# Kernel tuning notes

Hardware: AMD Instinct MI355X
Metric: run time of the kernel (lower is better)

The kernel has to match this reference:

```python
import jax, jax.numpy as jnp
import numpy as np

MODES = (16, 16, 16)

def setup_inputs() -> dict:
    key = jax.random.key(0)
    k1, k2, k3 = jax.random.split(key, 3)
    B, Cin, Cout = 4, 64, 64
    D = H = W = 64
    x = jax.random.normal(k1, (B, Cin, D, H, W), dtype=jnp.float32)
    weights = jax.random.normal(k2, (Cin, Cout) + MODES, dtype=jnp.float32) * (1.0 / (Cin * Cout)) ** 0.5
    bias = jax.random.normal(k3, (Cout,), dtype=jnp.float32)
    return {"x": x, "weights": weights, "bias": bias}


def reference(x, weights, bias):
    B = x.shape[0]
    Cout = weights.shape[1]
    spatial = x.shape[-3:]
    # 3D real FFT over last three dims -> (B, Cin, D, H, W//2+1) complex
    x_ft = jnp.fft.rfftn(x, axes=(-3, -2, -1))
    m1 = min(MODES[0], x_ft.shape[-3])
    m2 = min(MODES[1], x_ft.shape[-2])
    m3 = min(MODES[2], x_ft.shape[-1])
    # Per-mode channel mixing on truncated low-frequency block: one batched complex einsum
    mixed = jnp.einsum(
        'bixyz,ioxyz->boxyz',
        x_ft[:, :, :m1, :m2, :m3],
        weights[:, :, :m1, :m2, :m3],
    )
    out_ft = jnp.zeros((B, Cout) + x_ft.shape[2:], dtype=x_ft.dtype)
    out_ft = out_ft.at[:, :, :m1, :m2, :m3].set(mixed)
    x_out = jnp.fft.irfftn(out_ft, s=spatial, axes=(-3, -2, -1))
    return x_out + bias[None, :, None, None, None]
```

## Files before the change

### kernel.cpp

```cpp
#include <hip/hip_runtime.h>


#define ANG 0.09817477042468103f
#define C1W 0.9951847266721969f
#define S1W 0.0980171403295606f

__global__ __launch_bounds__(256) void k_fwd_hw(const float* __restrict__ x,
                                                float2* __restrict__ T1) {
  __shared__ float xs[64][68];
  __shared__ float2 irc[64][17];
  const int t = threadIdx.x;
  const int blk = blockIdx.x;
  const float* xg = x + (size_t)blk * 4096;
#pragma unroll
  for (int j = 0; j < 4; ++j) {
    int v = j * 256 + t;
    float4 val = reinterpret_cast<const float4*>(xg)[v];
    *reinterpret_cast<float4*>(&xs[v >> 4][(v & 15) * 4]) = val;
  }
  __syncthreads();
  {
    const int k = t & 15;
    const int g = t >> 4;
    float s1, c1;
    sincosf(ANG * (float)k, &s1, &c1);
    s1 = -s1;
    const float c2 = c1 * c1 - s1 * s1;
    const float s2 = 2.f * c1 * s1;
    float cw = 1.f, sw = 0.f;
    float ar0=0,ai0=0,ar1=0,ai1=0,ar2=0,ai2=0,ar3=0,ai3=0;
    const float2* r0 = reinterpret_cast<const float2*>(&xs[4*g+0][0]);
    const float2* r1 = reinterpret_cast<const float2*>(&xs[4*g+1][0]);
    const float2* r2 = reinterpret_cast<const float2*>(&xs[4*g+2][0]);
    const float2* r3 = reinterpret_cast<const float2*>(&xs[4*g+3][0]);
#pragma unroll 8
    for (int w2 = 0; w2 < 32; ++w2) {
      float2 v0 = r0[w2], v1 = r1[w2], v2 = r2[w2], v3 = r3[w2];
      float co = cw * c1 - sw * s1;
      float so = sw * c1 + cw * s1;
      ar0 = fmaf(v0.x, cw, ar0); ai0 = fmaf(v0.x, sw, ai0);
      ar1 = fmaf(v1.x, cw, ar1); ai1 = fmaf(v1.x, sw, ai1);
      ar2 = fmaf(v2.x, cw, ar2); ai2 = fmaf(v2.x, sw, ai2);
      ar3 = fmaf(v3.x, cw, ar3); ai3 = fmaf(v3.x, sw, ai3);
      ar0 = fmaf(v0.y, co, ar0); ai0 = fmaf(v0.y, so, ai0);
      ar1 = fmaf(v1.y, co, ar1); ai1 = fmaf(v1.y, so, ai1);
      ar2 = fmaf(v2.y, co, ar2); ai2 = fmaf(v2.y, so, ai2);
      ar3 = fmaf(v3.y, co, ar3); ai3 = fmaf(v3.y, so, ai3);
      float nc = cw * c2 - sw * s2;
      sw = sw * c2 + cw * s2;
      cw = nc;
    }
    irc[4*g+0][k] = make_float2(ar0, ai0);
    irc[4*g+1][k] = make_float2(ar1, ai1);
    irc[4*g+2][k] = make_float2(ar2, ai2);
    irc[4*g+3][k] = make_float2(ar3, ai3);
  }
  __syncthreads();
  {
    const int kz = t & 15, ky = t >> 4;
    float s1, c1;
    sincosf(ANG * (float)ky, &s1, &c1);
    s1 = -s1;
    float cw = 1.f, sw = 0.f, ar = 0.f, ai = 0.f;
#pragma unroll 8
    for (int r = 0; r < 64; ++r) {
      float2 v = irc[r][kz];
      ar += v.x * cw - v.y * sw;
      ai += v.y * cw + v.x * sw;
      float nc = cw * c1 - sw * s1;
      sw = sw * c1 + cw * s1;
      cw = nc;
    }
    T1[(size_t)blk * 256 + t] = make_float2(ar, ai);
  }
}

__global__ __launch_bounds__(256) void k_fwd_d(const float2* __restrict__ T1,
                                               float2* __restrict__ T2) {
  __shared__ float2 tw[64];
  const int t = threadIdx.x;
  if (t < 64) {
    float s, c; sincosf(ANG * (float)t, &s, &c);
    tw[t] = make_float2(c, s);
  }
  __syncthreads();
  const int bi = blockIdx.x;
  const float2* src = T1 + (size_t)bi * 16384 + t;
  float ar[16], ai[16];
#pragma unroll
  for (int q = 0; q < 16; ++q) { ar[q] = 0.f; ai[q] = 0.f; }
#pragma unroll 4
  for (int d = 0; d < 64; ++d) {
    float2 v = src[(size_t)d * 256];
    int m = 0;
#pragma unroll
    for (int kx = 0; kx < 16; ++kx) {
      float2 w = tw[m];
      ar[kx] = fmaf(v.x, w.x, fmaf(v.y, w.y, ar[kx]));
      ai[kx] = fmaf(v.y, w.x, fmaf(-v.x, w.y, ai[kx]));
      m = (m + d) & 63;
    }
  }
  float2* dst = T2 + (size_t)bi * 4096 + t;
#pragma unroll
  for (int kx = 0; kx < 16; ++kx)
    dst[(size_t)kx * 256] = make_float2(ar[kx], ai[kx]);
}

__global__ __launch_bounds__(256) void k_mix(const float2* __restrict__ T2,
                                             const float* __restrict__ wgt,
                                             float2* __restrict__ MX) {
  const int t = threadIdx.x;
  const int b = blockIdx.x >> 6;
  const int mode = ((blockIdx.x & 63) << 6) + (t & 63);
  const int og = t >> 6;
  const float2* xin = T2 + (size_t)b * 64 * 4096;
  float accr[16], acci[16];
#pragma unroll
  for (int j = 0; j < 16; ++j) { accr[j] = 0.f; acci[j] = 0.f; }
  for (int i = 0; i < 64; ++i) {
    float2 xv = xin[(size_t)i * 4096 + mode];
    const float* wp = wgt + ((size_t)i * 64 + og * 16) * 4096 + mode;
#pragma unroll
    for (int j = 0; j < 16; ++j) {
      float wv = wp[(size_t)j * 4096];
      accr[j] = fmaf(xv.x, wv, accr[j]);
      acci[j] = fmaf(xv.y, wv, acci[j]);
    }
  }
  float2* outp = MX + (size_t)b * 64 * 4096 + mode;
#pragma unroll
  for (int j = 0; j < 16; ++j)
    outp[(size_t)(og * 16 + j) * 4096] = make_float2(accr[j], acci[j]);
}

__global__ __launch_bounds__(256) void k_inv(const float2* __restrict__ MX,
                                             const float* __restrict__ bias,
                                             float* __restrict__ out) {
  __shared__ float2 tw[64];
  __shared__ float2 inb[16][17];
  __shared__ float2 g2[64][17];
  const int t = threadIdx.x;
  const int blk = blockIdx.x;
  const int d = blk & 63;
  const int bo = blk >> 6;
  if (t < 64) {
    float s, c; sincosf(ANG * (float)t, &s, &c);
    tw[t] = make_float2(c, s);
  }
  __syncthreads();
  {
    const float2* src = MX + (size_t)bo * 4096 + t;
    float ar = 0.f, ai = 0.f;
    int m = 0;
#pragma unroll
    for (int kx = 0; kx < 16; ++kx) {
      float2 v = src[(size_t)kx * 256];
      float2 w = tw[m];
      ar += v.x * w.x - v.y * w.y;
      ai += v.x * w.y + v.y * w.x;
      m = (m + d) & 63;
    }
    inb[t >> 4][t & 15] = make_float2(ar, ai);
  }
  __syncthreads();
  {
    const int kz = t & 15, g = t >> 4;
    const int h0 = 4 * g;
    float ar[4] = {0,0,0,0}, ai[4] = {0,0,0,0};
    int m0 = 0, m1 = 0, m2 = 0, m3 = 0;
#pragma unroll
    for (int ky = 0; ky < 16; ++ky) {
      float2 v = inb[ky][kz];
      float2 w0 = tw[m0], w1 = tw[m1], w2 = tw[m2], w3 = tw[m3];
      ar[0] += v.x*w0.x - v.y*w0.y; ai[0] += v.x*w0.y + v.y*w0.x;
      ar[1] += v.x*w1.x - v.y*w1.y; ai[1] += v.x*w1.y + v.y*w1.x;
      ar[2] += v.x*w2.x - v.y*w2.y; ai[2] += v.x*w2.y + v.y*w2.x;
      ar[3] += v.x*w3.x - v.y*w3.y; ai[3] += v.x*w3.y + v.y*w3.x;
      m0 = (m0 + h0    ) & 63; m1 = (m1 + h0 + 1) & 63;
      m2 = (m2 + h0 + 2) & 63; m3 = (m3 + h0 + 3) & 63;
    }
#pragma unroll
    for (int j = 0; j < 4; ++j)
      g2[h0 + j][kz] = make_float2(ar[j] + ar[j], ai[j] + ai[j]);
  }
  __syncthreads();
  {
    const int wq = t & 15, hg = t >> 4;
    const int w0 = wq * 4;
    float s0, c0;
    sincosf(ANG * (float)w0, &s0, &c0);
    float stc[4], sts[4];
    stc[0] = c0; sts[0] = s0;
    stc[1] = stc[0]*C1W - sts[0]*S1W; sts[1] = sts[0]*C1W + stc[0]*S1W;
    stc[2] = stc[1]*C1W - sts[1]*S1W; sts[2] = sts[1]*C1W + stc[1]*S1W;
    stc[3] = stc[2]*C1W - sts[2]*S1W; sts[3] = sts[2]*C1W + stc[2]*S1W;
    float chc[4], chs[4];
    float acc[4][4];
#pragma unroll
    for (int wi = 0; wi < 4; ++wi) { chc[wi] = stc[wi]; chs[wi] = sts[wi]; }
#pragma unroll
    for (int j = 0; j < 4; ++j) {
      float dc = 0.5f * g2[4*hg + j][0].x;
#pragma unroll
      for (int wi = 0; wi < 4; ++wi) acc[j][wi] = dc;
    }
#pragma unroll
    for (int kk = 1; kk < 16; ++kk) {
      float2 gv0 = g2[4*hg + 0][kk];
      float2 gv1 = g2[4*hg + 1][kk];
      float2 gv2 = g2[4*hg + 2][kk];
      float2 gv3 = g2[4*hg + 3][kk];
#pragma unroll
      for (int wi = 0; wi < 4; ++wi) {
        float c = chc[wi], s = chs[wi];
        acc[0][wi] = fmaf(gv0.x, c, fmaf(-gv0.y, s, acc[0][wi]));
        acc[1][wi] = fmaf(gv1.x, c, fmaf(-gv1.y, s, acc[1][wi]));
        acc[2][wi] = fmaf(gv2.x, c, fmaf(-gv2.y, s, acc[2][wi]));
        acc[3][wi] = fmaf(gv3.x, c, fmaf(-gv3.y, s, acc[3][wi]));
      }
#pragma unroll
      for (int wi = 0; wi < 4; ++wi) {
        float nc = chc[wi]*stc[wi] - chs[wi]*sts[wi];
        chs[wi] = chs[wi]*stc[wi] + chc[wi]*sts[wi];
        chc[wi] = nc;
      }
    }
    const float bv = bias[bo & 63];
    const float scale = 3.814697265625e-06f;
    float* og = out + (size_t)blk * 4096;
#pragma unroll
    for (int j = 0; j < 4; ++j) {
      float4 res;
      res.x = fmaf(acc[j][0], scale, bv);
      res.y = fmaf(acc[j][1], scale, bv);
      res.z = fmaf(acc[j][2], scale, bv);
      res.w = fmaf(acc[j][3], scale, bv);
      *reinterpret_cast<float4*>(og + (4*hg + j) * 64 + w0) = res;
    }
  }
}

extern "C" void kernel_launch(void* const* d_in, const int* in_sizes, int n_in,
                              void* d_out, int out_size, void* d_ws, size_t ws_size,
                              hipStream_t stream) {
  const float* x    = (const float*)d_in[0];
  const float* wgt  = (const float*)d_in[1];
  const float* bias = (const float*)d_in[2];
  float* out = (float*)d_out;

  float* wsf = (float*)d_ws;
  float2* T1 = (float2*)wsf;
  float2* T2 = (float2*)(wsf + 8388608);
  float2* MX = (float2*)(wsf + 8388608 + 2097152);

  k_fwd_hw<<<16384, 256, 0, stream>>>(x, T1);
  k_fwd_d <<<256,   256, 0, stream>>>(T1, T2);
  k_mix   <<<256,   256, 0, stream>>>(T2, wgt, MX);
  k_inv   <<<16384, 256, 0, stream>>>(MX, bias, out);
}
```

Baseline: 700.6 us.

## Restructure all four kernels with symmetry-folded DFTs and radix-4 splits

Result: faster. 647.8 us (-7.5%).

```diff
diff --git a/kernel.cpp b/kernel.cpp
--- a/kernel.cpp
+++ b/kernel.cpp
@@ -2,15 +2,18 @@
 
 
 #define ANG 0.09817477042468103f
-#define C1W 0.9951847266721969f
-#define S1W 0.0980171403295606f
 
 __global__ __launch_bounds__(256) void k_fwd_hw(const float* __restrict__ x,
                                                 float2* __restrict__ T1) {
   __shared__ float xs[64][68];
+  __shared__ float xpm[64][68];
   __shared__ float2 irc[64][17];
+  __shared__ float2 tw[64];
+  float2 (*U)[16][17] = reinterpret_cast<float2(*)[16][17]>(&xs[0][0]);
+
   const int t = threadIdx.x;
   const int blk = blockIdx.x;
+  if (t < 64) { float s, c; sincosf(ANG * (float)t, &s, &c); tw[t] = make_float2(c, s); }
   const float* xg = x + (size_t)blk * 4096;
 #pragma unroll
   for (int j = 0; j < 4; ++j) {
@@ -19,57 +22,79 @@
     *reinterpret_cast<float4*>(&xs[v >> 4][(v & 15) * 4]) = val;
   }
   __syncthreads();
-  {
-    const int k = t & 15;
-    const int g = t >> 4;
-    float s1, c1;
-    sincosf(ANG * (float)k, &s1, &c1);
-    s1 = -s1;
-    const float c2 = c1 * c1 - s1 * s1;
-    const float s2 = 2.f * c1 * s1;
-    float cw = 1.f, sw = 0.f;
-    float ar0=0,ai0=0,ar1=0,ai1=0,ar2=0,ai2=0,ar3=0,ai3=0;
-    const float2* r0 = reinterpret_cast<const float2*>(&xs[4*g+0][0]);
-    const float2* r1 = reinterpret_cast<const float2*>(&xs[4*g+1][0]);
-    const float2* r2 = reinterpret_cast<const float2*>(&xs[4*g+2][0]);
-    const float2* r3 = reinterpret_cast<const float2*>(&xs[4*g+3][0]);
-#pragma unroll 8
-    for (int w2 = 0; w2 < 32; ++w2) {
-      float2 v0 = r0[w2], v1 = r1[w2], v2 = r2[w2], v3 = r3[w2];
-      float co = cw * c1 - sw * s1;
-      float so = sw * c1 + cw * s1;
-      ar0 = fmaf(v0.x, cw, ar0); ai0 = fmaf(v0.x, sw, ai0);
-      ar1 = fmaf(v1.x, cw, ar1); ai1 = fmaf(v1.x, sw, ai1);
-      ar2 = fmaf(v2.x, cw, ar2); ai2 = fmaf(v2.x, sw, ai2);
-      ar3 = fmaf(v3.x, cw, ar3); ai3 = fmaf(v3.x, sw, ai3);
-      ar0 = fmaf(v0.y, co, ar0); ai0 = fmaf(v0.y, so, ai0);
-      ar1 = fmaf(v1.y, co, ar1); ai1 = fmaf(v1.y, so, ai1);
-      ar2 = fmaf(v2.y, co, ar2); ai2 = fmaf(v2.y, so, ai2);
-      ar3 = fmaf(v3.y, co, ar3); ai3 = fmaf(v3.y, so, ai3);
-      float nc = cw * c2 - sw * s2;
-      sw = sw * c2 + cw * s2;
-      cw = nc;
-    }
-    irc[4*g+0][k] = make_float2(ar0, ai0);
-    irc[4*g+1][k] = make_float2(ar1, ai1);
-    irc[4*g+2][k] = make_float2(ar2, ai2);
-    irc[4*g+3][k] = make_float2(ar3, ai3);
-  }
-  __syncthreads();
-  {
-    const int kz = t & 15, ky = t >> 4;
-    float s1, c1;
-    sincosf(ANG * (float)ky, &s1, &c1);
-    s1 = -s1;
-    float cw = 1.f, sw = 0.f, ar = 0.f, ai = 0.f;
-#pragma unroll 8
-    for (int r = 0; r < 64; ++r) {
-      float2 v = irc[r][kz];
-      ar += v.x * cw - v.y * sw;
-      ai += v.y * cw + v.x * sw;
-      float nc = cw * c1 - sw * s1;
-      sw = sw * c1 + cw * s1;
-      cw = nc;
+#pragma unroll
+  for (int p = 0; p < 8; ++p) {
+    int f = p * 256 + t;
+    int row = f >> 5, w = f & 31;
+    if (w == 0) { xpm[row][63] = xs[row][0]; xpm[row][64] = xs[row][32]; }
+    else {
+      float a = xs[row][w], b2 = xs[row][64 - w];
+      xpm[row][w - 1] = a + b2;
+      xpm[row][31 + w] = a - b2;
+    }
+  }
+  __syncthreads();
+  {
+    const int k = t & 15, g = t >> 4;
+    const int r0 = 4 * g;
+    const float x32sign = (k & 1) ? -1.f : 1.f;
+    float re[4], im[4];
+#pragma unroll
+    for (int j = 0; j < 4; ++j) {
+      re[j] = fmaf(x32sign, xpm[r0 + j][64], xpm[r0 + j][63]);
+      im[j] = 0.f;
+    }
+#pragma unroll 5
+    for (int i = 0; i < 15; ++i) {
+      int w = 2 * i + 1;
+      float2 tw1 = tw[(k * w) & 63];
+      float2 tw2 = tw[(k * (w + 1)) & 63];
+#pragma unroll
+      for (int j = 0; j < 4; ++j) {
+        float2 xp = *reinterpret_cast<const float2*>(&xpm[r0 + j][w - 1]);
+        float2 xm = *reinterpret_cast<const float2*>(&xpm[r0 + j][31 + w]);
+        re[j] = fmaf(xp.x, tw1.x, re[j]); im[j] = fmaf(xm.x, tw1.y, im[j]);
+        re[j] = fmaf(xp.y, tw2.x, re[j]); im[j] = fmaf(xm.y, tw2.y, im[j]);
+      }
+    }
+    {
+      float2 tw1 = tw[(k * 31) & 63];
+#pragma unroll
+      for (int j = 0; j < 4; ++j) {
+        re[j] = fmaf(xpm[r0 + j][30], tw1.x, re[j]);
+        im[j] = fmaf(xpm[r0 + j][62], tw1.y, im[j]);
+      }
+    }
+#pragma unroll
+    for (int j = 0; j < 4; ++j) irc[r0 + j][k] = make_float2(re[j], -im[j]);
+  }
+  __syncthreads();
+  {
+    const int rho = t >> 4, kz = t & 15;
+    float2 v0 = irc[rho][kz], v1 = irc[rho + 16][kz];
+    float2 v2 = irc[rho + 32][kz], v3 = irc[rho + 48][kz];
+    float t0r = v0.x + v2.x, t0i = v0.y + v2.y;
+    float t1r = v0.x - v2.x, t1i = v0.y - v2.y;
+    float t2r = v1.x + v3.x, t2i = v1.y + v3.y;
+    float t3r = v1.x - v3.x, t3i = v1.y - v3.y;
+    U[0][rho][kz] = make_float2(t0r + t2r, t0i + t2i);
+    U[2][rho][kz] = make_float2(t0r - t2r, t0i - t2i);
+    U[1][rho][kz] = make_float2(t1r + t3i, t1i - t3r);
+    U[3][rho][kz] = make_float2(t1r - t3i, t1i + t3r);
+  }
+  __syncthreads();
+  {
+    const int ky = t >> 4, kz = t & 15;
+    const int m = ky & 3;
+    float ar = 0.f, ai = 0.f;
+    int idx = 0;
+#pragma unroll
+    for (int rho = 0; rho < 16; ++rho) {
+      float2 wv = tw[idx];
+      float2 u = U[m][rho][kz];
+      ar = fmaf(u.x, wv.x, fmaf(u.y, wv.y, ar));
+      ai = fmaf(u.y, wv.x, fmaf(-u.x, wv.y, ai));
+      idx = (idx + ky) & 63;
     }
     T1[(size_t)blk * 256 + t] = make_float2(ar, ai);
   }
@@ -77,61 +102,71 @@
 
 __global__ __launch_bounds__(256) void k_fwd_d(const float2* __restrict__ T1,
                                                float2* __restrict__ T2) {
+  __shared__ float2 s1[64][17];
   __shared__ float2 tw[64];
   const int t = threadIdx.x;
-  if (t < 64) {
-    float s, c; sincosf(ANG * (float)t, &s, &c);
-    tw[t] = make_float2(c, s);
-  }
-  __syncthreads();
-  const int bi = blockIdx.x;
-  const float2* src = T1 + (size_t)bi * 16384 + t;
-  float ar[16], ai[16];
-#pragma unroll
-  for (int q = 0; q < 16; ++q) { ar[q] = 0.f; ai[q] = 0.f; }
-#pragma unroll 4
+  if (t < 64) { float s, c; sincosf(ANG * (float)t, &s, &c); tw[t] = make_float2(c, s); }
+  const int bi = blockIdx.x >> 4, ky = blockIdx.x & 15;
+  const float2* src = T1 + (size_t)bi * 16384 + ky * 16;
+#pragma unroll
+  for (int p = 0; p < 4; ++p) {
+    int j = p * 256 + t;
+    s1[j >> 4][j & 15] = src[(size_t)(j >> 4) * 256 + (j & 15)];
+  }
+  __syncthreads();
+  const int kx = t >> 4, kz = t & 15;
+  float ar = 0.f, ai = 0.f;
+  int idx = 0;
+#pragma unroll 8
   for (int d = 0; d < 64; ++d) {
-    float2 v = src[(size_t)d * 256];
-    int m = 0;
-#pragma unroll
-    for (int kx = 0; kx < 16; ++kx) {
-      float2 w = tw[m];
-      ar[kx] = fmaf(v.x, w.x, fmaf(v.y, w.y, ar[kx]));
-      ai[kx] = fmaf(v.y, w.x, fmaf(-v.x, w.y, ai[kx]));
-      m = (m + d) & 63;
-    }
-  }
-  float2* dst = T2 + (size_t)bi * 4096 + t;
-#pragma unroll
-  for (int kx = 0; kx < 16; ++kx)
-    dst[(size_t)kx * 256] = make_float2(ar[kx], ai[kx]);
+    float2 v = s1[d][kz];
+    float2 wv = tw[idx];
+    ar = fmaf(v.x, wv.x, fmaf(v.y, wv.y, ar));
+    ai = fmaf(v.y, wv.x, fmaf(-v.x, wv.y, ai));
+    idx = (idx + kx) & 63;
+  }
+  T2[(size_t)bi * 4096 + kx * 256 + ky * 16 + kz] = make_float2(ar, ai);
 }
 
 __global__ __launch_bounds__(256) void k_mix(const float2* __restrict__ T2,
                                              const float* __restrict__ wgt,
                                              float2* __restrict__ MX) {
-  const int t = threadIdx.x;
-  const int b = blockIdx.x >> 6;
-  const int mode = ((blockIdx.x & 63) << 6) + (t & 63);
-  const int og = t >> 6;
-  const float2* xin = T2 + (size_t)b * 64 * 4096;
-  float accr[16], acci[16];
-#pragma unroll
-  for (int j = 0; j < 16; ++j) { accr[j] = 0.f; acci[j] = 0.f; }
+  __shared__ float2 ts2[4][64][8];
+  const int t = threadIdx.x;
+  const int mbase = blockIdx.x * 8;
+#pragma unroll
+  for (int p = 0; p < 8; ++p) {
+    int j = p * 256 + t;
+    int m = j & 7, i = (j >> 3) & 63, b = j >> 9;
+    ts2[b][i][m] = T2[(size_t)(b * 64 + i) * 4096 + mbase + m];
+  }
+  __syncthreads();
+  const int b = t >> 6, o = t & 63;
+  float accr[8], acci[8];
+#pragma unroll
+  for (int m = 0; m < 8; ++m) { accr[m] = 0.f; acci[m] = 0.f; }
+  const float* wp0 = wgt + (size_t)o * 4096 + mbase;
+#pragma unroll 2
   for (int i = 0; i < 64; ++i) {
-    float2 xv = xin[(size_t)i * 4096 + mode];
-    const float* wp = wgt + ((size_t)i * 64 + og * 16) * 4096 + mode;
-#pragma unroll
-    for (int j = 0; j < 16; ++j) {
-      float wv = wp[(size_t)j * 4096];
-      accr[j] = fmaf(xv.x, wv, accr[j]);
-      acci[j] = fmaf(xv.y, wv, acci[j]);
-    }
-  }
-  float2* outp = MX + (size_t)b * 64 * 4096 + mode;
-#pragma unroll
-  for (int j = 0; j < 16; ++j)
-    outp[(size_t)(og * 16 + j) * 4096] = make_float2(accr[j], acci[j]);
+    const float* wp = wp0 + (size_t)i * 262144;
+    float4 wa = *reinterpret_cast<const float4*>(wp);
+    float4 wb = *reinterpret_cast<const float4*>(wp + 4);
+    const float4* xv = reinterpret_cast<const float4*>(&ts2[b][i][0]);
+    float4 x0 = xv[0], x1 = xv[1], x2 = xv[2], x3 = xv[3];
+    accr[0] = fmaf(x0.x, wa.x, accr[0]); acci[0] = fmaf(x0.y, wa.x, acci[0]);
+    accr[1] = fmaf(x0.z, wa.y, accr[1]); acci[1] = fmaf(x0.w, wa.y, acci[1]);
+    accr[2] = fmaf(x1.x, wa.z, accr[2]); acci[2] = fmaf(x1.y, wa.z, acci[2]);
+    accr[3] = fmaf(x1.z, wa.w, accr[3]); acci[3] = fmaf(x1.w, wa.w, acci[3]);
+    accr[4] = fmaf(x2.x, wb.x, accr[4]); acci[4] = fmaf(x2.y, wb.x, acci[4]);
+    accr[5] = fmaf(x2.z, wb.y, accr[5]); acci[5] = fmaf(x2.w, wb.y, acci[5]);
+    accr[6] = fmaf(x3.x, wb.z, accr[6]); acci[6] = fmaf(x3.y, wb.z, acci[6]);
+    accr[7] = fmaf(x3.z, wb.w, accr[7]); acci[7] = fmaf(x3.w, wb.w, acci[7]);
+  }
+  float4* outp = reinterpret_cast<float4*>(MX + (size_t)(b * 64 + o) * 4096 + mbase);
+  outp[0] = make_float4(accr[0], acci[0], accr[1], acci[1]);
+  outp[1] = make_float4(accr[2], acci[2], accr[3], acci[3]);
+  outp[2] = make_float4(accr[4], acci[4], accr[5], acci[5]);
+  outp[3] = make_float4(accr[6], acci[6], accr[7], acci[7]);
 }
 
 __global__ __launch_bounds__(256) void k_inv(const float2* __restrict__ MX,
@@ -142,101 +177,86 @@
   __shared__ float2 g2[64][17];
   const int t = threadIdx.x;
   const int blk = blockIdx.x;
-  const int d = blk & 63;
-  const int bo = blk >> 6;
-  if (t < 64) {
-    float s, c; sincosf(ANG * (float)t, &s, &c);
-    tw[t] = make_float2(c, s);
-  }
+  const int d = blk & 63, bo = blk >> 6;
+  if (t < 64) { float s, c; sincosf(ANG * (float)t, &s, &c); tw[t] = make_float2(c, s); }
   __syncthreads();
   {
     const float2* src = MX + (size_t)bo * 4096 + t;
     float ar = 0.f, ai = 0.f;
-    int m = 0;
+    int idx = 0;
 #pragma unroll
     for (int kx = 0; kx < 16; ++kx) {
       float2 v = src[(size_t)kx * 256];
-      float2 w = tw[m];
-      ar += v.x * w.x - v.y * w.y;
-      ai += v.x * w.y + v.y * w.x;
-      m = (m + d) & 63;
+      float2 wv = tw[idx];
+      ar = fmaf(v.x, wv.x, fmaf(-v.y, wv.y, ar));
+      ai = fmaf(v.x, wv.y, fmaf(v.y, wv.x, ai));
+      idx = (idx + d) & 63;
     }
     inb[t >> 4][t & 15] = make_float2(ar, ai);
   }
   __syncthreads();
   {
-    const int kz = t & 15, g = t >> 4;
-    const int h0 = 4 * g;
-    float ar[4] = {0,0,0,0}, ai[4] = {0,0,0,0};
-    int m0 = 0, m1 = 0, m2 = 0, m3 = 0;
+    const int j = t >> 4, kz = t & 15;
+    float2 S[4];
+#pragma unroll
+    for (int q = 0; q < 4; ++q) S[q] = make_float2(0.f, 0.f);
+    int idx = 0;
 #pragma unroll
     for (int ky = 0; ky < 16; ++ky) {
+      float2 wv = tw[idx];
       float2 v = inb[ky][kz];
-      float2 w0 = tw[m0], w1 = tw[m1], w2 = tw[m2], w3 = tw[m3];
-      ar[0] += v.x*w0.x - v.y*w0.y; ai[0] += v.x*w0.y + v.y*w0.x;
-      ar[1] += v.x*w1.x - v.y*w1.y; ai[1] += v.x*w1.y + v.y*w1.x;
-      ar[2] += v.x*w2.x - v.y*w2.y; ai[2] += v.x*w2.y + v.y*w2.x;
-      ar[3] += v.x*w3.x - v.y*w3.y; ai[3] += v.x*w3.y + v.y*w3.x;
-      m0 = (m0 + h0    ) & 63; m1 = (m1 + h0 + 1) & 63;
-      m2 = (m2 + h0 + 2) & 63; m3 = (m3 + h0 + 3) & 63;
-    }
-#pragma unroll
-    for (int j = 0; j < 4; ++j)
-      g2[h0 + j][kz] = make_float2(ar[j] + ar[j], ai[j] + ai[j]);
-  }
-  __syncthreads();
-  {
-    const int wq = t & 15, hg = t >> 4;
-    const int w0 = wq * 4;
-    float s0, c0;
-    sincosf(ANG * (float)w0, &s0, &c0);
-    float stc[4], sts[4];
-    stc[0] = c0; sts[0] = s0;
-    stc[1] = stc[0]*C1W - sts[0]*S1W; sts[1] = sts[0]*C1W + stc[0]*S1W;
-    stc[2] = stc[1]*C1W - sts[1]*S1W; sts[2] = sts[1]*C1W + stc[1]*S1W;
-    stc[3] = stc[2]*C1W - sts[2]*S1W; sts[3] = sts[2]*C1W + stc[2]*S1W;
-    float chc[4], chs[4];
-    float acc[4][4];
-#pragma unroll
-    for (int wi = 0; wi < 4; ++wi) { chc[wi] = stc[wi]; chs[wi] = sts[wi]; }
-#pragma unroll
-    for (int j = 0; j < 4; ++j) {
-      float dc = 0.5f * g2[4*hg + j][0].x;
-#pragma unroll
-      for (int wi = 0; wi < 4; ++wi) acc[j][wi] = dc;
-    }
-#pragma unroll
-    for (int kk = 1; kk < 16; ++kk) {
-      float2 gv0 = g2[4*hg + 0][kk];
-      float2 gv1 = g2[4*hg + 1][kk];
-      float2 gv2 = g2[4*hg + 2][kk];
-      float2 gv3 = g2[4*hg + 3][kk];
-#pragma unroll
-      for (int wi = 0; wi < 4; ++wi) {
-        float c = chc[wi], s = chs[wi];
-        acc[0][wi] = fmaf(gv0.x, c, fmaf(-gv0.y, s, acc[0][wi]));
-        acc[1][wi] = fmaf(gv1.x, c, fmaf(-gv1.y, s, acc[1][wi]));
-        acc[2][wi] = fmaf(gv2.x, c, fmaf(-gv2.y, s, acc[2][wi]));
-        acc[3][wi] = fmaf(gv3.x, c, fmaf(-gv3.y, s, acc[3][wi]));
-      }
-#pragma unroll
-      for (int wi = 0; wi < 4; ++wi) {
-        float nc = chc[wi]*stc[wi] - chs[wi]*sts[wi];
-        chs[wi] = chs[wi]*stc[wi] + chc[wi]*sts[wi];
-        chc[wi] = nc;
-      }
+      S[ky & 3].x = fmaf(v.x, wv.x, fmaf(-v.y, wv.y, S[ky & 3].x));
+      S[ky & 3].y = fmaf(v.x, wv.y, fmaf(v.y, wv.x, S[ky & 3].y));
+      idx = (idx + j) & 63;
+    }
+    float t0r = S[0].x + S[2].x, t0i = S[0].y + S[2].y;
+    float t1r = S[0].x - S[2].x, t1i = S[0].y - S[2].y;
+    float t2r = S[1].x + S[3].x, t2i = S[1].y + S[3].y;
+    float t3r = S[1].x - S[3].x, t3i = S[1].y - S[3].y;
+    float f = (kz == 0) ? 1.f : 2.f;
+    g2[j     ][kz] = make_float2(f * (t0r + t2r), f * (t0i + t2i));
+    g2[j + 16][kz] = make_float2(f * (t1r - t3i), f * (t1i + t3r));
+    g2[j + 32][kz] = make_float2(f * (t0r - t2r), f * (t0i - t2i));
+    g2[j + 48][kz] = make_float2(f * (t1r + t3i), f * (t1i - t3r));
+  }
+  __syncthreads();
+  {
+    const int b = t & 15, hg = t >> 4;
+    float twc[16], tws[16];
+    int idx = 0;
+#pragma unroll
+    for (int k = 0; k < 16; ++k) {
+      float2 wv = tw[idx];
+      twc[k] = wv.x; tws[k] = wv.y;
+      idx = (idx + b) & 63;
     }
     const float bv = bias[bo & 63];
     const float scale = 3.814697265625e-06f;
     float* og = out + (size_t)blk * 4096;
 #pragma unroll
-    for (int j = 0; j < 4; ++j) {
-      float4 res;
-      res.x = fmaf(acc[j][0], scale, bv);
-      res.y = fmaf(acc[j][1], scale, bv);
-      res.z = fmaf(acc[j][2], scale, bv);
-      res.w = fmaf(acc[j][3], scale, bv);
-      *reinterpret_cast<float4*>(og + (4*hg + j) * 64 + w0) = res;
+    for (int j2 = 0; j2 < 4; ++j2) {
+      const int h = 4 * hg + j2;
+      float S0r = 0.f, S2r = 0.f, S1r = 0.f, S1i = 0.f, S3r = 0.f, S3i = 0.f;
+#pragma unroll
+      for (int k = 0; k < 16; ++k) {
+        float2 g = g2[h][k];
+        float pr = fmaf(g.x, twc[k], -g.y * tws[k]);
+        if ((k & 1) == 0) {
+          if ((k & 3) == 0) S0r += pr; else S2r += pr;
+        } else {
+          float pi = fmaf(g.x, tws[k], g.y * twc[k]);
+          if ((k & 3) == 1) { S1r += pr; S1i += pi; }
+          else              { S3r += pr; S3i += pi; }
+        }
+      }
+      float e0 = S0r + S2r;
+      float e1 = S0r - S2r;
+      float e2 = S1r + S3r;
+      float e3 = S1i - S3i;
+      og[h * 64 + b     ] = fmaf(e0 + e2, scale, bv);
+      og[h * 64 + b + 16] = fmaf(e1 - e3, scale, bv);
+      og[h * 64 + b + 32] = fmaf(e0 - e2, scale, bv);
+      og[h * 64 + b + 48] = fmaf(e1 + e3, scale, bv);
     }
   }
 }
@@ -255,7 +275,7 @@
   float2* MX = (float2*)(wsf + 8388608 + 2097152);
 
   k_fwd_hw<<<16384, 256, 0, stream>>>(x, T1);
-  k_fwd_d <<<256,   256, 0, stream>>>(T1, T2);
-  k_mix   <<<256,   256, 0, stream>>>(T2, wgt, MX);
+  k_fwd_d <<<4096,  256, 0, stream>>>(T1, T2);
+  k_mix   <<<512,   256, 0, stream>>>(T2, wgt, MX);
   k_inv   <<<16384, 256, 0, stream>>>(MX, bias, out);
 }
```
